# Kernel optimization log

Measured on AMD Instinct MI355X. Metric: run time of the kernel, lower is better.

The kernel has to match this reference:

```python
import jax, jax.numpy as jnp
import numpy as np

D_MODEL = 1024
N_HEADS = 16
D_K = D_MODEL // N_HEADS


def setup_inputs() -> dict:
    key = jax.random.key(0)
    ks = jax.random.split(key, 10)
    B, S = 4, 2048
    scale = 1.0 / np.sqrt(D_MODEL)
    inp = {
        "x": jax.random.normal(ks[0], (B, S, D_MODEL), dtype=jnp.float32),
        "mask": jnp.ones((B, S), dtype=jnp.int32),
        "w_q": jax.random.normal(ks[1], (D_MODEL, D_MODEL), dtype=jnp.float32) * scale,
        "b_q": jnp.zeros((D_MODEL,), dtype=jnp.float32),
        "w_k": jax.random.normal(ks[2], (D_MODEL, D_MODEL), dtype=jnp.float32) * scale,
        "b_k": jnp.zeros((D_MODEL,), dtype=jnp.float32),
        "w_v": jax.random.normal(ks[3], (D_MODEL, D_MODEL), dtype=jnp.float32) * scale,
        "b_v": jnp.zeros((D_MODEL,), dtype=jnp.float32),
        "w_o": jax.random.normal(ks[4], (D_MODEL, D_MODEL), dtype=jnp.float32) * scale,
        "b_o": jnp.zeros((D_MODEL,), dtype=jnp.float32),
    }
    return inp


def reference(x, mask, w_q, b_q, w_k, b_k, w_v, b_v, w_o, b_o):
    B, S, _ = x.shape
    # projections; weights stored (in, out) so x @ W + b
    def proj(w, b):
        return (x @ w + b).reshape(B, S, N_HEADS, D_K).transpose(0, 2, 1, 3)  # [B,H,S,Dk]
    Q = proj(w_q, b_q)
    K = proj(w_k, b_k)
    V = proj(w_v, b_v)
    scores = jnp.einsum("bhqd,bhkd->bhqk", Q, K) / np.sqrt(D_K)  # [B,H,S,S]
    # mask: (B,S) -> (B,1,1,S); masked positions set to -1e9 (matches masked_fill)
    scores = jnp.where(mask[:, None, None, :] == 0, jnp.float32(-1e9), scores)
    attn = jax.nn.softmax(scores, axis=-1)
    # dropout is identity at inference (eval mode)
    context = jnp.einsum("bhqk,bhkd->bhqd", attn, V)  # [B,H,S,Dk]
    context = context.transpose(0, 2, 1, 3).reshape(B, S, D_MODEL)
    return context @ w_o + b_o
```

## Files before the change

### kernel.cpp

```cpp
#include <hip/hip_runtime.h>

typedef __attribute__((ext_vector_type(8)))  short short8;
typedef __attribute__((ext_vector_type(4)))  float f32x4;
typedef __attribute__((ext_vector_type(16))) float f32x16;

__device__ __forceinline__ short f2b(float f) {
    union { float f; unsigned u; } v; v.f = f;
    unsigned r = v.u + 0x7FFF + ((v.u >> 16) & 1);
    return (short)(r >> 16);
}

__device__ __forceinline__ float fexp2(float x) {
    float r;
    asm("v_exp_f32 %0, %1" : "=v"(r) : "v"(x));
    return r;
}

__device__ __forceinline__ unsigned cvtpk(float a, float b) {
    unsigned r;
    asm("v_cvt_pk_bf16_f32 %0, %1, %2" : "=v"(r) : "v"(a), "v"(b));
    return r;
}

__device__ __forceinline__ void plswap(unsigned &a, unsigned &b) {
    asm("v_permlane32_swap_b32 %0, %1" : "+v"(a), "+v"(b));
}

__device__ __forceinline__ void gll16(const void* g, void* l) {
    __builtin_amdgcn_global_load_lds(
        (const __attribute__((address_space(1))) void*)g,
        (__attribute__((address_space(3))) void*)l, 16, 0, 0);
}


__global__ __launch_bounds__(256) void xconv_kernel(const float4* __restrict__ X,
                                                    short* __restrict__ xb) {
    int i = blockIdx.x * 256 + threadIdx.x;
    float4 v = X[i];
    short4 o;
    o.x = f2b(v.x); o.y = f2b(v.y); o.z = f2b(v.z); o.w = f2b(v.w);
    ((short4*)xb)[i] = o;
}

__global__ __launch_bounds__(256) void wconv4_kernel(
    const float* __restrict__ w0, const float* __restrict__ w1,
    const float* __restrict__ w2, const float* __restrict__ w3,
    short* __restrict__ wqkvt, short* __restrict__ wot) {
    __shared__ float t[32][33];
    int z = blockIdx.z;
    const float* W = (z == 0) ? w0 : (z == 1) ? w1 : (z == 2) ? w2 : w3;
    short* WT = (z < 3) ? wqkvt : wot;
    int row_off = (z < 3) ? z * 1024 : 0;
    int bx = blockIdx.x, by = blockIdx.y;
    int c = threadIdx.x & 31, r0 = threadIdx.x >> 5;
    #pragma unroll
    for (int p = 0; p < 4; ++p) {
        int r = r0 + p * 8;
        t[r][c] = W[(size_t)(by * 32 + r) * 1024 + bx * 32 + c];
    }
    __syncthreads();
    #pragma unroll
    for (int p = 0; p < 4; ++p) {
        int r = r0 + p * 8;
        WT[(size_t)(row_off + bx * 32 + r) * 1024 + by * 32 + c] = f2b(t[c][r]);
    }
}

__global__ __launch_bounds__(256) void vtrans_kernel(const short* __restrict__ V,
                                                     short* __restrict__ Vt) {
    __shared__ short t[64][72];
    int st = blockIdx.x, bh = blockIdx.y;
    const size_t vbase = (size_t)bh * 2048 * 64;
    const size_t tbase = (size_t)bh * 64 * 2048;
    int tid = threadIdx.x;
    #pragma unroll
    for (int p = 0; p < 16; ++p) {
        int e = p * 256 + tid;
        int r = e >> 6, c = e & 63;
        t[r][c] = V[vbase + (size_t)(st * 64 + r) * 64 + c];
    }
    __syncthreads();
    #pragma unroll
    for (int p = 0; p < 16; ++p) {
        int e = p * 256 + tid;
        int d = e >> 6, c = e & 63;
        Vt[tbase + (size_t)d * 2048 + st * 64 + c] = t[c][d];
    }
}

__global__ __launch_bounds__(256) void mfma_gemm_kernel(
    const short* __restrict__ A, const short* __restrict__ Bt,
    const float* __restrict__ b0, const float* __restrict__ b1,
    const float* __restrict__ b2,
    short* __restrict__ Qo, short* __restrict__ Ko, short* __restrict__ Vo,
    float* __restrict__ Co, int K, int mode)
{
    __shared__ __align__(16) short As[2][128 * 32];
    __shared__ __align__(16) short Bs[2][128 * 32];

    const int tid = threadIdx.x;
    const int lane = tid & 63;
    const int w = tid >> 6;
    const int quad = lane >> 4;
    const int l15 = lane & 15;
    const int wm = (w & 1) * 64;
    const int wn = (w >> 1) * 64;
    const int m0 = blockIdx.y * 128;
    const int n0 = blockIdx.x * 128;

    const int rl = lane >> 2;
    const int cl = lane & 3;
    const short* srcA[2]; const short* srcB[2];
    int doff[2];
    #pragma unroll
    for (int t = 0; t < 2; ++t) {
        int row = w * 32 + t * 16 + rl;
        int sc = cl ^ (row & 3);
        srcA[t] = A  + (size_t)(m0 + row) * K + sc * 8;
        srcB[t] = Bt + (size_t)(n0 + row) * K + sc * 8;
        doff[t] = (w * 32 + t * 16) * 32;
    }

    int offA[4], offB[4];
    #pragma unroll
    for (int i = 0; i < 4; ++i) {
        int m = wm + i * 16 + l15;
        offA[i] = m * 32 + ((quad ^ (m & 3)) * 8);
        int n = wn + i * 16 + l15;
        offB[i] = n * 32 + ((quad ^ (n & 3)) * 8);
    }

    f32x4 acc[4][4];
    #pragma unroll
    for (int i = 0; i < 4; ++i)
        #pragma unroll
        for (int j = 0; j < 4; ++j)
            acc[i][j] = (f32x4){0.f, 0.f, 0.f, 0.f};

    #pragma unroll
    for (int t = 0; t < 2; ++t) {
        gll16(srcA[t], As[0] + doff[t]);
        gll16(srcB[t], Bs[0] + doff[t]);
    }
    __syncthreads();

    const int KT = K >> 5;
    for (int kt = 0; kt < KT; ++kt) {
        if (kt + 1 < KT) {
            int k1 = (kt + 1) << 5;
            int nb = (kt + 1) & 1;
            #pragma unroll
            for (int t = 0; t < 2; ++t) {
                gll16(srcA[t] + k1, As[nb] + doff[t]);
                gll16(srcB[t] + k1, Bs[nb] + doff[t]);
            }
        }
        const short* as = As[kt & 1];
        const short* bs = Bs[kt & 1];
        short8 af[4], bfr[4];
        #pragma unroll
        for (int i = 0; i < 4; ++i) af[i] = *(const short8*)(as + offA[i]);
        #pragma unroll
        for (int j = 0; j < 4; ++j) bfr[j] = *(const short8*)(bs + offB[j]);
        #pragma unroll
        for (int i = 0; i < 4; ++i)
            #pragma unroll
            for (int j = 0; j < 4; ++j)
                acc[i][j] = __builtin_amdgcn_mfma_f32_16x16x32_bf16(af[i], bfr[j], acc[i][j], 0, 0, 0);
        __syncthreads();
    }

    #pragma unroll
    for (int j = 0; j < 4; ++j) {
        int ng = n0 + wn + j * 16 + l15;
        if (mode == 0) {
            int mat = ng >> 10;
            int nl = ng & 1023;
            float bv = (mat == 0) ? b0[nl] : (mat == 1) ? b1[nl] : b2[nl];
            short* dst = (mat == 0) ? Qo : (mat == 1) ? Ko : Vo;
            float scl = (mat == 0) ? 0.18033688011112042f : 1.0f;
            int hh = nl >> 6, dd = nl & 63;
            #pragma unroll
            for (int i = 0; i < 4; ++i)
                #pragma unroll
                for (int r = 0; r < 4; ++r) {
                    int mg = m0 + wm + i * 16 + quad * 4 + r;
                    int bb = mg >> 11, ss = mg & 2047;
                    dst[(((size_t)(bb * 16 + hh)) * 2048 + ss) * 64 + dd] = f2b((acc[i][j][r] + bv) * scl);
                }
        } else {
            float bv = b0[ng];
            #pragma unroll
            for (int i = 0; i < 4; ++i)
                #pragma unroll
                for (int r = 0; r < 4; ++r) {
                    int mg = m0 + wm + i * 16 + quad * 4 + r;
                    Co[(size_t)mg * 1024 + ng] = acc[i][j][r] + bv;
                }
        }
    }
}

__global__ __launch_bounds__(256) void attn_mfma_kernel(
    const short* __restrict__ Q, const short* __restrict__ Kg,
    const short* __restrict__ Vt, const int* __restrict__ mask,
    short* __restrict__ ctx)
{
    __shared__ __align__(16) short Ks[2][64 * 64];
    __shared__ __align__(16) short Vs[2][64 * 64];
    __shared__ int msks[2][64];
    __shared__ float Linv[4][32];

    const int tid = threadIdx.x;
    const int lane = tid & 63;
    const int w = tid >> 6;
    const int l31 = lane & 31;
    const int hi = lane >> 5;
    const int bh = blockIdx.x;
    const int q0 = blockIdx.y * 128;
    const int h = bh & 15;
    const int b = bh >> 4;
    const size_t qkbase = (size_t)bh * 2048 * 64;
    const size_t vtbase = (size_t)bh * 64 * 2048;

    const int rl8 = lane >> 3;
    const int cl8 = lane & 7;

    const short* srcK[2]; const short* srcV[2];
    int dstoff[2];
    #pragma unroll
    for (int t = 0; t < 2; ++t) {
        int row = w * 16 + t * 8 + rl8;
        int sc = cl8 ^ (row & 7);
        srcK[t] = Kg + qkbase + (size_t)row * 64 + sc * 8;
        srcV[t] = Vt + vtbase + (size_t)row * 2048 + sc * 8;
        dstoff[t] = (w * 16 + t * 8) * 64;
    }

    #pragma unroll
    for (int t = 0; t < 2; ++t) {
        gll16(srcK[t], Ks[0] + dstoff[t]);
        gll16(srcV[t], Vs[0] + dstoff[t]);
    }
    if (tid < 64) msks[0][tid] = mask[b * 2048 + tid];

    short8 qf[4];
    {
        const short* qptr = Q + qkbase + (size_t)(q0 + w * 32 + l31) * 64;
        #pragma unroll
        for (int s = 0; s < 4; ++s)
            qf[s] = *(const short8*)(qptr + (((s << 1) | hi)) * 8);
    }

    f32x16 zz;
    #pragma unroll
    for (int r = 0; r < 16; ++r) zz[r] = 0.f;

    f32x16 o[2];
    #pragma unroll
    for (int ch = 0; ch < 2; ++ch)
        #pragma unroll
        for (int r = 0; r < 16; ++r) o[ch][r] = 0.f;
    float lq[4];
    #pragma unroll
    for (int c = 0; c < 4; ++c) lq[c] = 0.f;

    __syncthreads();

    for (int t = 0; t < 32; ++t) {
        const int bidx = t & 1;
        if (t + 1 < 32) {
            const int nb = (t + 1) & 1;
            const int kt1 = (t + 1) * 64;
            #pragma unroll
            for (int s = 0; s < 2; ++s) {
                gll16(srcK[s] + (size_t)kt1 * 64, Ks[nb] + dstoff[s]);
                gll16(srcV[s] + kt1, Vs[nb] + dstoff[s]);
            }
            if (tid < 64) msks[nb][tid] = mask[b * 2048 + kt1 + tid];
        }

        const short* ks = Ks[bidx];
        const short* vs = Vs[bidx];
        unsigned long long bz = __ballot(msks[bidx][lane] == 0);

        #pragma unroll
        for (int km = 0; km < 2; ++km) {
            const int kr = km * 32 + l31;
            short8 ka0 = *(const short8*)(ks + kr * 64 + ((hi ^ (l31 & 7))) * 8);
            f32x16 sa = __builtin_amdgcn_mfma_f32_32x32x16_bf16(ka0, qf[0], zz, 0, 0, 0);
            #pragma unroll
            for (int s = 1; s < 4; ++s) {
                short8 ka = *(const short8*)(ks + kr * 64 + (((s << 1) | hi) ^ (l31 & 7)) * 8);
                sa = __builtin_amdgcn_mfma_f32_32x32x16_bf16(ka, qf[s], sa, 0, 0, 0);
            }
            float ps[16];
            #pragma unroll
            for (int r = 0; r < 16; ++r) ps[r] = fexp2(sa[r]);
            if (bz) {
                #pragma unroll
                for (int r = 0; r < 16; ++r) {
                    int key = km * 32 + (r & 3) + 8 * (r >> 2) + 4 * hi;
                    if (msks[bidx][key] == 0) ps[r] = 0.f;
                }
            }
            #pragma unroll
            for (int c = 0; c < 4; ++c)
                lq[c] += ((ps[4 * c] + ps[4 * c + 1]) + (ps[4 * c + 2] + ps[4 * c + 3]));

            unsigned p0 = cvtpk(ps[0],  ps[1]);
            unsigned p1 = cvtpk(ps[2],  ps[3]);
            unsigned p2 = cvtpk(ps[4],  ps[5]);
            unsigned p3 = cvtpk(ps[6],  ps[7]);
            unsigned p4 = cvtpk(ps[8],  ps[9]);
            unsigned p5 = cvtpk(ps[10], ps[11]);
            unsigned p6 = cvtpk(ps[12], ps[13]);
            unsigned p7 = cvtpk(ps[14], ps[15]);
            plswap(p0, p2);
            plswap(p1, p3);
            plswap(p4, p6);
            plswap(p5, p7);

            uint4 A1u, A2u;
            A1u.x = p0; A1u.y = p1; A1u.z = p2; A1u.w = p3;
            A2u.x = p4; A2u.y = p5; A2u.z = p6; A2u.w = p7;
            short8 A1 = __builtin_bit_cast(short8, A1u);
            short8 A2 = __builtin_bit_cast(short8, A2u);

            #pragma unroll
            for (int ch = 0; ch < 2; ++ch) {
                const int d = ch * 32 + l31;
                short8 vb0 = *(const short8*)(vs + d * 64 + (((km * 4) | hi) ^ (d & 7)) * 8);
                short8 vb1 = *(const short8*)(vs + d * 64 + (((km * 4 + 2) | hi) ^ (d & 7)) * 8);
                o[ch] = __builtin_amdgcn_mfma_f32_32x32x16_bf16(A1, vb0, o[ch], 0, 0, 0);
                o[ch] = __builtin_amdgcn_mfma_f32_32x32x16_bf16(A2, vb1, o[ch], 0, 0, 0);
            }
        }
        __syncthreads();
    }

    float lsum = (lq[0] + lq[1]) + (lq[2] + lq[3]);
    float ltot = lsum + __shfl_xor(lsum, 32);
    if (hi == 0) Linv[w][l31] = 1.0f / ltot;
    asm volatile("s_waitcnt lgkmcnt(0)" ::: "memory");
    float invr[16];
    #pragma unroll
    for (int r = 0; r < 16; ++r)
        invr[r] = Linv[w][(r & 3) + 8 * (r >> 2) + 4 * hi];
    #pragma unroll
    for (int ch = 0; ch < 2; ++ch)
        #pragma unroll
        for (int r = 0; r < 16; ++r) {
            int rowq = (r & 3) + 8 * (r >> 2) + 4 * hi;
            int qg = q0 + w * 32 + rowq;
            ctx[((size_t)b * 2048 + qg) * 1024 + h * 64 + ch * 32 + l31] =
                f2b(o[ch][r] * invr[r]);
        }
}


extern "C" void kernel_launch(void* const* d_in, const int* in_sizes, int n_in,
                              void* d_out, int out_size, void* d_ws, size_t ws_size,
                              hipStream_t stream) {
    const size_t ME = (size_t)8192 * 1024;

    char* ws = (char*)d_ws;
    short* xb    = (short*)ws; ws += ME * 2;
    short* wqkvt = (short*)ws; ws += (size_t)3072 * 1024 * 2;
    short* wot   = (short*)ws; ws += (size_t)1024 * 1024 * 2;
    short* Qb    = (short*)ws; ws += ME * 2;
    short* Kb    = (short*)ws; ws += ME * 2;
    short* Vb    = (short*)ws; ws += ME * 2;
    short* Vt    = (short*)ws; ws += ME * 2;

    xconv_kernel<<<8192, 256, 0, stream>>>((const float4*)d_in[0], xb);
    wconv4_kernel<<<dim3(32, 32, 4), 256, 0, stream>>>(
        (const float*)d_in[2], (const float*)d_in[4],
        (const float*)d_in[6], (const float*)d_in[8], wqkvt, wot);

    mfma_gemm_kernel<<<dim3(24, 64), 256, 0, stream>>>(
        xb, wqkvt, (const float*)d_in[3], (const float*)d_in[5], (const float*)d_in[7],
        Qb, Kb, Vb, nullptr, 1024, 0);

    vtrans_kernel<<<dim3(32, 64), 256, 0, stream>>>(Vb, Vt);

    attn_mfma_kernel<<<dim3(64, 16), 256, 0, stream>>>(
        Qb, Kb, Vt, (const int*)d_in[1], xb );

    mfma_gemm_kernel<<<dim3(8, 64), 256, 0, stream>>>(
        xb, wot, (const float*)d_in[9], nullptr, nullptr,
        nullptr, nullptr, nullptr, (float*)d_out, 1024, 1);
}
```

Measured before the change: 317.3 us.

## Process two 128-row query tiles per attention block to reuse K/V tiles

Each attention workgroup now handles 256 query rows (two interleaved 128-row sub-tiles A and B), so every K/V tile loaded into LDS feeds twice as many MFMAs. The grid is halved to 64x8 blocks. This cuts K/V global and LDS traffic per unit of work and interleaves independent MFMA chains for better latency hiding. The cost is roughly double the accumulator and score registers, which may lower occupancy, and fewer blocks (512) to spread across the CUs.

```diff
diff --git a/kernel.cpp b/kernel.cpp
--- a/kernel.cpp
+++ b/kernel.cpp
@@ -209,7 +209,8 @@
     __shared__ __align__(16) short Ks[2][64 * 64];
     __shared__ __align__(16) short Vs[2][64 * 64];
     __shared__ int msks[2][64];
-    __shared__ float Linv[4][32];
+    __shared__ float LinvA[4][32];
+    __shared__ float LinvB[4][32];
 
     const int tid = threadIdx.x;
     const int lane = tid & 63;
@@ -217,7 +218,7 @@
     const int l31 = lane & 31;
     const int hi = lane >> 5;
     const int bh = blockIdx.x;
-    const int q0 = blockIdx.y * 128;
+    const int q0 = blockIdx.y * 256;
     const int h = bh & 15;
     const int b = bh >> 4;
     const size_t qkbase = (size_t)bh * 2048 * 64;
@@ -244,26 +245,29 @@
     }
     if (tid < 64) msks[0][tid] = mask[b * 2048 + tid];
 
-    short8 qf[4];
+    short8 qfa[4], qfb[4];
     {
-        const short* qptr = Q + qkbase + (size_t)(q0 + w * 32 + l31) * 64;
-        #pragma unroll
-        for (int s = 0; s < 4; ++s)
-            qf[s] = *(const short8*)(qptr + (((s << 1) | hi)) * 8);
+        const short* qptrA = Q + qkbase + (size_t)(q0 + w * 32 + l31) * 64;
+        const short* qptrB = qptrA + 128 * 64;
+        #pragma unroll
+        for (int s = 0; s < 4; ++s) {
+            qfa[s] = *(const short8*)(qptrA + (((s << 1) | hi)) * 8);
+            qfb[s] = *(const short8*)(qptrB + (((s << 1) | hi)) * 8);
+        }
     }
 
     f32x16 zz;
     #pragma unroll
     for (int r = 0; r < 16; ++r) zz[r] = 0.f;
 
-    f32x16 o[2];
+    f32x16 oa[2], ob[2];
     #pragma unroll
     for (int ch = 0; ch < 2; ++ch)
         #pragma unroll
-        for (int r = 0; r < 16; ++r) o[ch][r] = 0.f;
-    float lq[4];
-    #pragma unroll
-    for (int c = 0; c < 4; ++c) lq[c] = 0.f;
+        for (int r = 0; r < 16; ++r) { oa[ch][r] = 0.f; ob[ch][r] = 0.f; }
+    float lqa[4], lqb[4];
+    #pragma unroll
+    for (int c = 0; c < 4; ++c) { lqa[c] = 0.f; lqb[c] = 0.f; }
 
     __syncthreads();
 
@@ -288,73 +292,103 @@
         for (int km = 0; km < 2; ++km) {
             const int kr = km * 32 + l31;
             short8 ka0 = *(const short8*)(ks + kr * 64 + ((hi ^ (l31 & 7))) * 8);
-            f32x16 sa = __builtin_amdgcn_mfma_f32_32x32x16_bf16(ka0, qf[0], zz, 0, 0, 0);
-            #pragma unroll
-            for (int s = 1; s < 4; ++s) {
-                short8 ka = *(const short8*)(ks + kr * 64 + (((s << 1) | hi) ^ (l31 & 7)) * 8);
-                sa = __builtin_amdgcn_mfma_f32_32x32x16_bf16(ka, qf[s], sa, 0, 0, 0);
-            }
-            float ps[16];
-            #pragma unroll
-            for (int r = 0; r < 16; ++r) ps[r] = fexp2(sa[r]);
+            short8 ka1 = *(const short8*)(ks + kr * 64 + (((2 | hi)) ^ (l31 & 7)) * 8);
+            short8 ka2 = *(const short8*)(ks + kr * 64 + (((4 | hi)) ^ (l31 & 7)) * 8);
+            short8 ka3 = *(const short8*)(ks + kr * 64 + (((6 | hi)) ^ (l31 & 7)) * 8);
+            f32x16 saA = __builtin_amdgcn_mfma_f32_32x32x16_bf16(ka0, qfa[0], zz, 0, 0, 0);
+            f32x16 saB = __builtin_amdgcn_mfma_f32_32x32x16_bf16(ka0, qfb[0], zz, 0, 0, 0);
+            saA = __builtin_amdgcn_mfma_f32_32x32x16_bf16(ka1, qfa[1], saA, 0, 0, 0);
+            saB = __builtin_amdgcn_mfma_f32_32x32x16_bf16(ka1, qfb[1], saB, 0, 0, 0);
+            saA = __builtin_amdgcn_mfma_f32_32x32x16_bf16(ka2, qfa[2], saA, 0, 0, 0);
+            saB = __builtin_amdgcn_mfma_f32_32x32x16_bf16(ka2, qfb[2], saB, 0, 0, 0);
+            saA = __builtin_amdgcn_mfma_f32_32x32x16_bf16(ka3, qfa[3], saA, 0, 0, 0);
+            saB = __builtin_amdgcn_mfma_f32_32x32x16_bf16(ka3, qfb[3], saB, 0, 0, 0);
+
+            float psA[16], psB[16];
+            #pragma unroll
+            for (int r = 0; r < 16; ++r) { psA[r] = fexp2(saA[r]); psB[r] = fexp2(saB[r]); }
             if (bz) {
                 #pragma unroll
                 for (int r = 0; r < 16; ++r) {
                     int key = km * 32 + (r & 3) + 8 * (r >> 2) + 4 * hi;
-                    if (msks[bidx][key] == 0) ps[r] = 0.f;
+                    if (msks[bidx][key] == 0) { psA[r] = 0.f; psB[r] = 0.f; }
                 }
             }
             #pragma unroll
-            for (int c = 0; c < 4; ++c)
-                lq[c] += ((ps[4 * c] + ps[4 * c + 1]) + (ps[4 * c + 2] + ps[4 * c + 3]));
-
-            unsigned p0 = cvtpk(ps[0],  ps[1]);
-            unsigned p1 = cvtpk(ps[2],  ps[3]);
-            unsigned p2 = cvtpk(ps[4],  ps[5]);
-            unsigned p3 = cvtpk(ps[6],  ps[7]);
-            unsigned p4 = cvtpk(ps[8],  ps[9]);
-            unsigned p5 = cvtpk(ps[10], ps[11]);
-            unsigned p6 = cvtpk(ps[12], ps[13]);
-            unsigned p7 = cvtpk(ps[14], ps[15]);
-            plswap(p0, p2);
-            plswap(p1, p3);
-            plswap(p4, p6);
-            plswap(p5, p7);
-
-            uint4 A1u, A2u;
-            A1u.x = p0; A1u.y = p1; A1u.z = p2; A1u.w = p3;
-            A2u.x = p4; A2u.y = p5; A2u.z = p6; A2u.w = p7;
-            short8 A1 = __builtin_bit_cast(short8, A1u);
-            short8 A2 = __builtin_bit_cast(short8, A2u);
+            for (int c = 0; c < 4; ++c) {
+                lqa[c] += ((psA[4 * c] + psA[4 * c + 1]) + (psA[4 * c + 2] + psA[4 * c + 3]));
+                lqb[c] += ((psB[4 * c] + psB[4 * c + 1]) + (psB[4 * c + 2] + psB[4 * c + 3]));
+            }
+
+            unsigned a0 = cvtpk(psA[0],  psA[1]);
+            unsigned a1 = cvtpk(psA[2],  psA[3]);
+            unsigned a2 = cvtpk(psA[4],  psA[5]);
+            unsigned a3 = cvtpk(psA[6],  psA[7]);
+            unsigned a4 = cvtpk(psA[8],  psA[9]);
+            unsigned a5 = cvtpk(psA[10], psA[11]);
+            unsigned a6 = cvtpk(psA[12], psA[13]);
+            unsigned a7 = cvtpk(psA[14], psA[15]);
+            plswap(a0, a2); plswap(a1, a3); plswap(a4, a6); plswap(a5, a7);
+            uint4 A1au, A2au;
+            A1au.x = a0; A1au.y = a1; A1au.z = a2; A1au.w = a3;
+            A2au.x = a4; A2au.y = a5; A2au.z = a6; A2au.w = a7;
+            short8 A1a = __builtin_bit_cast(short8, A1au);
+            short8 A2a = __builtin_bit_cast(short8, A2au);
+
+            unsigned g0 = cvtpk(psB[0],  psB[1]);
+            unsigned g1 = cvtpk(psB[2],  psB[3]);
+            unsigned g2 = cvtpk(psB[4],  psB[5]);
+            unsigned g3 = cvtpk(psB[6],  psB[7]);
+            unsigned g4 = cvtpk(psB[8],  psB[9]);
+            unsigned g5 = cvtpk(psB[10], psB[11]);
+            unsigned g6 = cvtpk(psB[12], psB[13]);
+            unsigned g7 = cvtpk(psB[14], psB[15]);
+            plswap(g0, g2); plswap(g1, g3); plswap(g4, g6); plswap(g5, g7);
+            uint4 B1u, B2u;
+            B1u.x = g0; B1u.y = g1; B1u.z = g2; B1u.w = g3;
+            B2u.x = g4; B2u.y = g5; B2u.z = g6; B2u.w = g7;
+            short8 A1b = __builtin_bit_cast(short8, B1u);
+            short8 A2b = __builtin_bit_cast(short8, B2u);
 
             #pragma unroll
             for (int ch = 0; ch < 2; ++ch) {
                 const int d = ch * 32 + l31;
                 short8 vb0 = *(const short8*)(vs + d * 64 + (((km * 4) | hi) ^ (d & 7)) * 8);
                 short8 vb1 = *(const short8*)(vs + d * 64 + (((km * 4 + 2) | hi) ^ (d & 7)) * 8);
-                o[ch] = __builtin_amdgcn_mfma_f32_32x32x16_bf16(A1, vb0, o[ch], 0, 0, 0);
-                o[ch] = __builtin_amdgcn_mfma_f32_32x32x16_bf16(A2, vb1, o[ch], 0, 0, 0);
+                oa[ch] = __builtin_amdgcn_mfma_f32_32x32x16_bf16(A1a, vb0, oa[ch], 0, 0, 0);
+                ob[ch] = __builtin_amdgcn_mfma_f32_32x32x16_bf16(A1b, vb0, ob[ch], 0, 0, 0);
+                oa[ch] = __builtin_amdgcn_mfma_f32_32x32x16_bf16(A2a, vb1, oa[ch], 0, 0, 0);
+                ob[ch] = __builtin_amdgcn_mfma_f32_32x32x16_bf16(A2b, vb1, ob[ch], 0, 0, 0);
             }
         }
         __syncthreads();
     }
 
-    float lsum = (lq[0] + lq[1]) + (lq[2] + lq[3]);
-    float ltot = lsum + __shfl_xor(lsum, 32);
-    if (hi == 0) Linv[w][l31] = 1.0f / ltot;
+    float lsumA = (lqa[0] + lqa[1]) + (lqa[2] + lqa[3]);
+    float ltotA = lsumA + __shfl_xor(lsumA, 32);
+    float lsumB = (lqb[0] + lqb[1]) + (lqb[2] + lqb[3]);
+    float ltotB = lsumB + __shfl_xor(lsumB, 32);
+    if (hi == 0) {
+        LinvA[w][l31] = 1.0f / ltotA;
+        LinvB[w][l31] = 1.0f / ltotB;
+    }
     asm volatile("s_waitcnt lgkmcnt(0)" ::: "memory");
-    float invr[16];
-    #pragma unroll
-    for (int r = 0; r < 16; ++r)
-        invr[r] = Linv[w][(r & 3) + 8 * (r >> 2) + 4 * hi];
+    float invrA[16], invrB[16];
+    #pragma unroll
+    for (int r = 0; r < 16; ++r) {
+        int rowq = (r & 3) + 8 * (r >> 2) + 4 * hi;
+        invrA[r] = LinvA[w][rowq];
+        invrB[r] = LinvB[w][rowq];
+    }
     #pragma unroll
     for (int ch = 0; ch < 2; ++ch)
         #pragma unroll
         for (int r = 0; r < 16; ++r) {
             int rowq = (r & 3) + 8 * (r >> 2) + 4 * hi;
             int qg = q0 + w * 32 + rowq;
-            ctx[((size_t)b * 2048 + qg) * 1024 + h * 64 + ch * 32 + l31] =
-                f2b(o[ch][r] * invr[r]);
+            size_t base = ((size_t)b * 2048 + qg) * 1024 + h * 64 + ch * 32 + l31;
+            ctx[base] = f2b(oa[ch][r] * invrA[r]);
+            ctx[base + (size_t)128 * 1024] = f2b(ob[ch][r] * invrB[r]);
         }
 }
 
@@ -384,7 +418,7 @@
 
     vtrans_kernel<<<dim3(32, 64), 256, 0, stream>>>(Vb, Vt);
 
-    attn_mfma_kernel<<<dim3(64, 16), 256, 0, stream>>>(
+    attn_mfma_kernel<<<dim3(64, 8), 256, 0, stream>>>(
         Qb, Kb, Vt, (const int*)d_in[1], xb );
 
     mfma_gemm_kernel<<<dim3(8, 64), 256, 0, stream>>>(
```

Measured after the change: 304.5 us. 1.04x faster.
